# Optimization experiments

Hardware: AMD Instinct MI355X
Metric: run time of the kernel (lower is better)

The kernel has to match this reference:

```python
import jax, jax.numpy as jnp
import numpy as np
import math

B, H, S, D = 2, 16, 2048, 64

def setup_inputs() -> dict:
    key = jax.random.key(0)
    kq, kk, kv, km = jax.random.split(key, 4)
    query = jax.random.normal(kq, (B, H, S, D), dtype=jnp.float32)
    k_ = jax.random.normal(kk, (B, H, S, D), dtype=jnp.float32)
    value = jax.random.normal(kv, (B, H, S, D), dtype=jnp.float32)
    mask = jax.random.randint(km, (B, 1, 1, S), 0, 2, dtype=jnp.int32)
    return {"query": query, "key": k_, "value": value, "mask": mask}

def reference(query, key, value, mask):
    # scores: [B,H,S,S] = QK^T / sqrt(D)
    scale = 1.0 / math.sqrt(query.shape[-1])
    scores = jnp.einsum('bhqd,bhkd->bhqk', query, key) * scale
    # masked_fill(mask == 0, -1e9); mask broadcasts [B,1,1,S] -> [B,H,S,S]
    scores = jnp.where(mask == 0, jnp.float32(-1e9), scores)
    p_attn = jax.nn.softmax(scores, axis=-1)
    out = jnp.einsum('bhqk,bhkd->bhqd', p_attn, value)
    return (out, p_attn)
```

## Files before the change

kernel.cpp:

```cpp
#include <hip/hip_runtime.h>
#include <cstdint>
#include <cstddef>


typedef float f32x4 __attribute__((ext_vector_type(4)));
typedef short s16x8 __attribute__((ext_vector_type(8)));
typedef unsigned int u32;

#define S_LEN 2048
#define D_DIM 64
#define NKT   32
#define QSCALE 0.18033688011112042f

__device__ __forceinline__ unsigned short f2bf(float f) {
  unsigned u = __builtin_bit_cast(unsigned, f);
  u += 0x7FFFu + ((u >> 16) & 1u);
  return (unsigned short)(u >> 16);
}

__device__ __forceinline__ f32x4 mfma16(s16x8 a, s16x8 b, f32x4 c) {
  return __builtin_amdgcn_mfma_f32_16x16x32_bf16(a, b, c, 0, 0, 0);
}

__device__ __forceinline__ void gl_lds16(const void* g, void* l) {
  __builtin_amdgcn_global_load_lds(
      (const __attribute__((address_space(1))) u32*)g,
      (__attribute__((address_space(3))) u32*)l, 16, 0, 0);
}


__global__ void prep_k(const float* __restrict__ Kg, unsigned short* __restrict__ kb) {
  const int kt = blockIdx.x, bh = blockIdx.y, tid = threadIdx.x;
  const int r = tid >> 2, c0 = (tid & 3) << 4;
  const float* src = Kg + (((size_t)bh * S_LEN) + kt * 64 + r) * D_DIM + c0;
  f32x4 f0 = *(const f32x4*)(src);
  f32x4 f1 = *(const f32x4*)(src + 4);
  f32x4 f2 = *(const f32x4*)(src + 8);
  f32x4 f3 = *(const f32x4*)(src + 12);
  s16x8 h0, h1;
#pragma unroll
  for (int j = 0; j < 4; j++) {
    h0[j] = (short)f2bf(f0[j]); h0[j + 4] = (short)f2bf(f1[j]);
    h1[j] = (short)f2bf(f2[j]); h1[j + 4] = (short)f2bf(f3[j]);
  }
  char* dst = (char*)(kb + ((size_t)bh * 32 + kt) * 4096);
  const int swz = (r & 7) << 4;
  *(s16x8*)(dst + (r << 7) + (((c0 << 1) + 0)  ^ swz)) = h0;
  *(s16x8*)(dst + (r << 7) + (((c0 << 1) + 16) ^ swz)) = h1;
}

__global__ void prep_v(const float* __restrict__ Vg, unsigned short* __restrict__ vb) {
  __shared__ float tv[64 * 65];
  const int kt = blockIdx.x, bh = blockIdx.y, tid = threadIdx.x;
  const int r = tid >> 2, c0 = (tid & 3) << 4;
  const float* src = Vg + (((size_t)bh * S_LEN) + kt * 64 + r) * D_DIM + c0;
#pragma unroll
  for (int j = 0; j < 4; j++)
    *(f32x4*)(tv + r * 65 + c0 + j * 4) = *(const f32x4*)(src + j * 4);
  __syncthreads();
  const int d = tid >> 2, k0 = (tid & 3) << 4;
  s16x8 h0, h1;
#pragma unroll
  for (int j = 0; j < 8; j++) {
    h0[j] = (short)f2bf(tv[(k0 + j) * 65 + d]);
    h1[j] = (short)f2bf(tv[(k0 + 8 + j) * 65 + d]);
  }
  char* dst = (char*)(vb + ((size_t)bh * 32 + kt) * 4096);
  const int swz = (d & 7) << 4;
  *(s16x8*)(dst + (d << 7) + (((k0 << 1) + 0)  ^ swz)) = h0;
  *(s16x8*)(dst + (d << 7) + (((k0 << 1) + 16) ^ swz)) = h1;
}


__global__ __launch_bounds__(512, 4) void attn_main(
    const float* __restrict__ Qg, const unsigned short* __restrict__ Kb,
    const unsigned short* __restrict__ Vb, const int* __restrict__ Mg,
    float* __restrict__ Og, float* __restrict__ Pg)
{
  __shared__ __align__(16) short s_kv[4][4096];
  __shared__ __align__(16) short s_vv[4][4096];
  __shared__ __align__(16) short s_p[8][1024];

  const int tid = threadIdx.x;
  const int w = tid >> 6, l = tid & 63, lo = l & 15, hi = l >> 4;
  const int wg = blockIdx.x;
  const int bh = (wg & 7) * 4 + ((wg >> 3) >> 4);
  const int qt = (wg >> 3) & 15;
  const int b = bh >> 4;
  const int ph = wg & 31;

  unsigned* mbuild = (unsigned*)s_p;
  if (tid < 64) mbuild[tid] = 0u;
  __syncthreads();
  {
    const int4 mv = *(const int4*)(Mg + b * S_LEN + tid * 4);
    unsigned nib = (mv.x ? 1u : 0u) | (mv.y ? 2u : 0u) |
                   (mv.z ? 4u : 0u) | (mv.w ? 8u : 0u);
    atomicOr(&mbuild[tid >> 3], nib << ((tid & 7) * 4));
  }
  __syncthreads();
  const unsigned mword = mbuild[l];
  __syncthreads();

  const size_t bhS = (size_t)bh * S_LEN;
  const int q0w = qt * 128 + w * 16;

  const float* qsrc = Qg + (bhS + q0w + lo) * D_DIM + hi * 8;
  s16x8 bq0, bq1;
  {
    f32x4 a0 = *(const f32x4*)(qsrc);
    f32x4 a1 = *(const f32x4*)(qsrc + 4);
    f32x4 c0 = *(const f32x4*)(qsrc + 32);
    f32x4 c1 = *(const f32x4*)(qsrc + 36);
#pragma unroll
    for (int j = 0; j < 4; j++) {
      bq0[j]     = (short)f2bf(a0[j] * QSCALE);
      bq0[j + 4] = (short)f2bf(a1[j] * QSCALE);
      bq1[j]     = (short)f2bf(c0[j] * QSCALE);
      bq1[j + 4] = (short)f2bf(c1[j] * QSCALE);
    }
  }

  const char* ktile = (const char*)(Kb + bhS * D_DIM);
  const char* vtile = (const char*)(Vb + bhS * D_DIM);
  char* ldsk = (char*)s_kv;
  char* ldsv = (char*)s_vv;
  char* pb  = (char*)s_p[w];
  const int swz = (lo & 7) << 4;
  const int hs  = hi << 2;

  gl_lds16(ktile + ((0 + ph) & 31) * 8192 + tid * 16, ldsk + 0 * 8192 + tid * 16);
  gl_lds16(ktile + ((1 + ph) & 31) * 8192 + tid * 16, ldsk + 1 * 8192 + tid * 16);

  float lacc[4] = {0.f, 0.f, 0.f, 0.f};
  for (int j = 0; j < 16; j++) {
    const int h = j & 1;
    asm volatile("s_waitcnt vmcnt(0)" ::: "memory");
    __builtin_amdgcn_s_barrier();
    __builtin_amdgcn_sched_barrier(0);
    if (j < 15) {
      gl_lds16(ktile + ((2 * j + 2 + ph) & 31) * 8192 + tid * 16,
               ldsk + (2 * (h ^ 1)) * 8192 + tid * 16);
      gl_lds16(ktile + ((2 * j + 3 + ph) & 31) * 8192 + tid * 16,
               ldsk + (2 * (h ^ 1) + 1) * 8192 + tid * 16);
    }
#pragma unroll
    for (int t2 = 0; t2 < 2; t2++) {
      const int t = (2 * j + t2 + ph) & 31;
      const char* kc = ldsk + (2 * h + t2) * 8192;
      f32x4 acc[4] = {};
#pragma unroll
      for (int nn = 0; nn < 4; nn++) {
        const int rb = (nn * 16 + lo) << 7;
        s16x8 ka0 = *(const s16x8*)(kc + rb + ((0 + hi * 16) ^ swz));
        s16x8 ka1 = *(const s16x8*)(kc + rb + ((64 + hi * 16) ^ swz));
        acc[nn] = mfma16(ka0, bq0, acc[nn]);
        acc[nn] = mfma16(ka1, bq1, acc[nn]);
      }
      const unsigned w0 = (unsigned)__shfl((int)mword, 2 * t);
      const unsigned w1 = (unsigned)__shfl((int)mword, 2 * t + 1);
#pragma unroll
      for (int nn = 0; nn < 4; nn++) {
        const unsigned m4 = (((nn & 2) ? w1 : w0) >> (((nn & 1) << 4) + hs)) & 0xF;
#pragma unroll
        for (int r = 0; r < 4; r++) {
          const float e = exp2f(acc[nn][r]);
          lacc[nn] += ((m4 >> r) & 1) ? e : 0.0f;
        }
      }
    }
  }
  float lsum = (lacc[0] + lacc[1]) + (lacc[2] + lacc[3]);
  lsum += __shfl_xor(lsum, 16, 64);
  lsum += __shfl_xor(lsum, 32, 64);
  const float inv = 1.0f / lsum;

  __syncthreads();

  gl_lds16(ktile + ((0 + ph) & 31) * 8192 + tid * 16, ldsk + 0 * 8192 + tid * 16);
  gl_lds16(ktile + ((1 + ph) & 31) * 8192 + tid * 16, ldsk + 1 * 8192 + tid * 16);
  gl_lds16(vtile + ((0 + ph) & 31) * 8192 + tid * 16, ldsv + 0 * 8192 + tid * 16);
  gl_lds16(vtile + ((1 + ph) & 31) * 8192 + tid * 16, ldsv + 1 * 8192 + tid * 16);

  f32x4 oacc[4] = {};
  for (int j = 0; j < 16; j++) {
    const int h = j & 1;
    if (j == 0) asm volatile("s_waitcnt vmcnt(0)" ::: "memory");
    else        asm volatile("s_waitcnt vmcnt(8)" ::: "memory");
    __builtin_amdgcn_s_barrier();
    __builtin_amdgcn_sched_barrier(0);
    if (j < 15) {
      gl_lds16(ktile + ((2 * j + 2 + ph) & 31) * 8192 + tid * 16,
               ldsk + (2 * (h ^ 1)) * 8192 + tid * 16);
      gl_lds16(ktile + ((2 * j + 3 + ph) & 31) * 8192 + tid * 16,
               ldsk + (2 * (h ^ 1) + 1) * 8192 + tid * 16);
      gl_lds16(vtile + ((2 * j + 2 + ph) & 31) * 8192 + tid * 16,
               ldsv + (2 * (h ^ 1)) * 8192 + tid * 16);
      gl_lds16(vtile + ((2 * j + 3 + ph) & 31) * 8192 + tid * 16,
               ldsv + (2 * (h ^ 1) + 1) * 8192 + tid * 16);
    }
#pragma unroll
    for (int t2 = 0; t2 < 2; t2++) {
      const int t = (2 * j + t2 + ph) & 31;
      const char* kc = ldsk + (2 * h + t2) * 8192;
      const char* vc = ldsv + (2 * h + t2) * 8192;

      f32x4 acc[4] = {};
#pragma unroll
      for (int nn = 0; nn < 4; nn++) {
        const int rb = (nn * 16 + lo) << 7;
        s16x8 ka0 = *(const s16x8*)(kc + rb + ((0 + hi * 16) ^ swz));
        s16x8 ka1 = *(const s16x8*)(kc + rb + ((64 + hi * 16) ^ swz));
        acc[nn] = mfma16(ka0, bq0, acc[nn]);
        acc[nn] = mfma16(ka1, bq1, acc[nn]);
      }
      const unsigned w0 = (unsigned)__shfl((int)mword, 2 * t);
      const unsigned w1 = (unsigned)__shfl((int)mword, 2 * t + 1);
      const int colb = t * 64;
      float* prow = Pg + (bhS + q0w + lo) * S_LEN + colb;
#pragma unroll
      for (int nn = 0; nn < 4; nn++) {
        const unsigned m4 = (((nn & 2) ? w1 : w0) >> (((nn & 1) << 4) + hs)) & 0xF;
        f32x4 p;
#pragma unroll
        for (int r = 0; r < 4; r++) {
          const float e = exp2f(acc[nn][r]) * inv;
          p[r] = ((m4 >> r) & 1) ? e : 0.0f;
        }
        *(f32x4*)(prow + nn * 16 + hi * 4) = p;
        unsigned d0, d1;
        asm("v_cvt_pk_bf16_f32 %0, %1, %2" : "=v"(d0) : "v"(p[0]), "v"(p[1]));
        asm("v_cvt_pk_bf16_f32 %0, %1, %2" : "=v"(d1) : "v"(p[2]), "v"(p[3]));
        *(unsigned long long*)(pb + (lo << 7) + ((nn * 32 + hi * 8) ^ swz)) =
            ((unsigned long long)d1 << 32) | d0;
      }
#pragma unroll
      for (int kk2 = 0; kk2 < 2; kk2++) {
        s16x8 bp = *(const s16x8*)(pb + (lo << 7) + ((kk2 * 64 + hi * 16) ^ swz));
#pragma unroll
        for (int dd = 0; dd < 4; dd++) {
          s16x8 va = *(const s16x8*)(vc + ((dd * 16 + lo) << 7) +
                                     ((kk2 * 64 + hi * 16) ^ swz));
          oacc[dd] = mfma16(va, bp, oacc[dd]);
        }
      }
    }
  }
#pragma unroll
  for (int dd = 0; dd < 4; dd++)
    *(f32x4*)(Og + (bhS + q0w + lo) * D_DIM + dd * 16 + hi * 4) = oacc[dd];
}


__device__ __forceinline__ void stage_k(const float* __restrict__ g, char* lb, int tid) {
  const int kr = tid >> 2;
  const int c0 = (tid & 3) << 4;
  const f32x4* src = (const f32x4*)(g + kr * D_DIM + c0);
  f32x4 f0 = src[0], f1 = src[1], f2 = src[2], f3 = src[3];
  s16x8 h0, h1;
#pragma unroll
  for (int j = 0; j < 4; j++) {
    h0[j] = (short)f2bf(f0[j]); h0[j + 4] = (short)f2bf(f1[j]);
    h1[j] = (short)f2bf(f2[j]); h1[j + 4] = (short)f2bf(f3[j]);
  }
  const int base = kr << 7;
  const int swz = (kr & 7) << 4;
  *(s16x8*)(lb + base + (((c0 << 1) + 0) ^ swz)) = h0;
  *(s16x8*)(lb + base + (((c0 << 1) + 16) ^ swz)) = h1;
}

__device__ __forceinline__ void stage_v(const float* __restrict__ g, char* lb, int tid) {
  const int k0 = (tid >> 3) << 1;
  const int c0 = (tid & 7) << 3;
  const f32x4* s0 = (const f32x4*)(g + k0 * D_DIM + c0);
  const f32x4* s1 = (const f32x4*)(g + (k0 + 1) * D_DIM + c0);
  f32x4 a0 = s0[0], a1 = s0[1];
  f32x4 b0 = s1[0], b1 = s1[1];
  const int kc = (k0 >> 3) & 7;
  const int kb2 = (k0 & 7) << 1;
#pragma unroll
  for (int j = 0; j < 8; j++) {
    float fa = (j < 4) ? a0[j & 3] : a1[j & 3];
    float fb = (j < 4) ? b0[j & 3] : b1[j & 3];
    unsigned u = (unsigned)f2bf(fa) | ((unsigned)f2bf(fb) << 16);
    const int d = c0 + j;
    const int off = (d << 7) + (((kc ^ j ^ (d >> 3)) & 7) << 4) + kb2;
    *(unsigned*)(lb + off) = u;
  }
}

__global__ __launch_bounds__(256, 4) void attn_fwd(
    const float* __restrict__ Qg, const float* __restrict__ Kg,
    const float* __restrict__ Vg, const int* __restrict__ Mg,
    float* __restrict__ Og, float* __restrict__ Pg)
{
  __shared__ __align__(16) float s_bias[S_LEN];
  __shared__ __align__(16) short s_k[64 * 64];
  __shared__ __align__(16) short s_v[64 * 64];
  __shared__ __align__(16) short s_p[4 * 16 * 64];

  const int tid = threadIdx.x;
  const int w = tid >> 6, l = tid & 63, lo = l & 15, hi = l >> 4;
  const int bh = blockIdx.x, qt = blockIdx.y, b = bh >> 4;

  for (int i = tid; i < S_LEN; i += 256)
    s_bias[i] = Mg[b * S_LEN + i] ? 0.0f : -INFINITY;

  const int q0 = qt * 64 + w * 16;
  const float* qptr = Qg + ((size_t)bh * S_LEN + q0 + lo) * D_DIM + hi * 8;
  s16x8 aq[2];
#pragma unroll
  for (int kk = 0; kk < 2; kk++) {
    f32x4 v0 = *(const f32x4*)(qptr + kk * 32);
    f32x4 v1 = *(const f32x4*)(qptr + kk * 32 + 4);
#pragma unroll
    for (int j = 0; j < 4; j++) {
      aq[kk][j] = (short)f2bf(v0[j] * QSCALE);
      aq[kk][j + 4] = (short)f2bf(v1[j] * QSCALE);
    }
  }
  char* kb = (char*)s_k;
  char* vb = (char*)s_v;
  char* pb = (char*)s_p + (w << 11);
  const size_t bhS = (size_t)bh * S_LEN;
  __syncthreads();

  float lsum[4] = {0.f, 0.f, 0.f, 0.f};
  for (int kt = 0; kt < NKT; kt++) {
    stage_k(Kg + (bhS + kt * 64) * D_DIM, kb, tid);
    __syncthreads();
    f32x4 acc[4] = {};
#pragma unroll
    for (int kk = 0; kk < 2; kk++)
#pragma unroll
      for (int nn = 0; nn < 4; nn++) {
        const int row = nn * 16 + lo;
        s16x8 bk = *(const s16x8*)(kb + (row << 7) +
                     ((kk * 64 + hi * 16) ^ ((row & 7) << 4)));
        acc[nn] = mfma16(aq[kk], bk, acc[nn]);
      }
    const int colb = kt * 64;
#pragma unroll
    for (int nn = 0; nn < 4; nn++) {
      const float bias = s_bias[colb + nn * 16 + lo];
#pragma unroll
      for (int r = 0; r < 4; r++)
        lsum[r] += exp2f(acc[nn][r] + bias);
    }
    __syncthreads();
  }
#pragma unroll
  for (int r = 0; r < 4; r++)
#pragma unroll
    for (int off = 1; off < 16; off <<= 1)
      lsum[r] += __shfl_xor(lsum[r], off, 64);
  float inv[4];
#pragma unroll
  for (int r = 0; r < 4; r++) inv[r] = 1.0f / lsum[r];

  f32x4 oacc[4] = {};
  const int qd0 = q0 + hi * 4;
  for (int kt = 0; kt < NKT; kt++) {
    stage_k(Kg + (bhS + kt * 64) * D_DIM, kb, tid);
    stage_v(Vg + (bhS + kt * 64) * D_DIM, vb, tid);
    __syncthreads();
    f32x4 acc[4] = {};
#pragma unroll
    for (int kk = 0; kk < 2; kk++)
#pragma unroll
      for (int nn = 0; nn < 4; nn++) {
        const int row = nn * 16 + lo;
        s16x8 bk = *(const s16x8*)(kb + (row << 7) +
                     ((kk * 64 + hi * 16) ^ ((row & 7) << 4)));
        acc[nn] = mfma16(aq[kk], bk, acc[nn]);
      }
    const int colb = kt * 64;
#pragma unroll
    for (int nn = 0; nn < 4; nn++) {
      const int col = colb + nn * 16 + lo;
      const float bias = s_bias[col];
#pragma unroll
      for (int r = 0; r < 4; r++) {
        const float p = exp2f(acc[nn][r] + bias) * inv[r];
        Pg[(bhS + (size_t)(qd0 + r)) * S_LEN + col] = p;
        const int prow = hi * 4 + r;
        *(unsigned short*)(pb + (prow << 7) +
            ((((nn * 16 + lo) << 1)) ^ ((prow & 7) << 4))) = f2bf(p);
      }
    }
#pragma unroll
    for (int kk2 = 0; kk2 < 2; kk2++) {
      s16x8 ap = *(const s16x8*)(pb + (lo << 7) +
                   ((kk2 * 64 + hi * 16) ^ ((lo & 7) << 4)));
#pragma unroll
      for (int dd = 0; dd < 4; dd++) {
        const int d = dd * 16 + lo;
        const int chunk = ((kk2 * 4 + hi) ^ (d & 7) ^ (d >> 3)) & 7;
        s16x8 bv = *(const s16x8*)(vb + (d << 7) + (chunk << 4));
        oacc[dd] = mfma16(ap, bv, oacc[dd]);
      }
    }
    __syncthreads();
  }
#pragma unroll
  for (int dd = 0; dd < 4; dd++)
#pragma unroll
    for (int r = 0; r < 4; r++)
      Og[(bhS + (size_t)(qd0 + r)) * D_DIM + dd * 16 + lo] = oacc[dd][r];
}

extern "C" void kernel_launch(void* const* d_in, const int* in_sizes, int n_in,
                              void* d_out, int out_size, void* d_ws, size_t ws_size,
                              hipStream_t stream) {
  const float* Q = (const float*)d_in[0];
  const float* K = (const float*)d_in[1];
  const float* V = (const float*)d_in[2];
  const int*   M = (const int*)d_in[3];
  float* out = (float*)d_out;
  float* P = out + (size_t)2 * 16 * 2048 * 64;

  const size_t elems = (size_t)2 * 16 * 2048 * 64;
  if (ws_size >= elems * 2 * sizeof(unsigned short)) {
    unsigned short* kb = (unsigned short*)d_ws;
    unsigned short* vb = kb + elems;
    prep_k<<<dim3(32, 32), 256, 0, stream>>>(K, kb);
    prep_v<<<dim3(32, 32), 256, 0, stream>>>(V, vb);
    attn_main<<<dim3(512), 512, 0, stream>>>(Q, kb, vb, M, out, P);
  } else {
    attn_fwd<<<dim3(32, 32), dim3(256), 0, stream>>>(Q, K, V, M, out, P);
  }
}
```

Measured before the change: 177.7 us.

## Halve workgroup to 4 waves, each wave computing 32 query rows

The attention kernel now launches 256 threads per block instead of 512. Each wave handles 32 query rows (two 16-row MFMA tiles) instead of 16, so every K/V fragment read from LDS is reused across twice as many MFMAs. The K/V staging issues two global-to-LDS loads per thread per tile, the mask bitfield build is adapted, and the vmcnt wait counts are raised to match. In exchange there are fewer waves per block to hide latency and register pressure per wave goes up.

```diff
diff --git a/kernel.cpp b/kernel.cpp
--- a/kernel.cpp
+++ b/kernel.cpp
@@ -72,14 +72,25 @@
 }
 
 
-__global__ __launch_bounds__(512, 4) void attn_main(
+#define KSTAGE(t, buf) do { \
+    gl_lds16(ktile + (size_t)(t) * 8192 + tid * 16, \
+             ldsk + (buf) * 8192 + tid * 16); \
+    gl_lds16(ktile + (size_t)(t) * 8192 + 4096 + tid * 16, \
+             ldsk + (buf) * 8192 + 4096 + tid * 16); } while (0)
+#define VSTAGE(t, buf) do { \
+    gl_lds16(vtile + (size_t)(t) * 8192 + tid * 16, \
+             ldsv + (buf) * 8192 + tid * 16); \
+    gl_lds16(vtile + (size_t)(t) * 8192 + 4096 + tid * 16, \
+             ldsv + (buf) * 8192 + 4096 + tid * 16); } while (0)
+
+__global__ __launch_bounds__(256, 2) void attn_main(
     const float* __restrict__ Qg, const unsigned short* __restrict__ Kb,
     const unsigned short* __restrict__ Vb, const int* __restrict__ Mg,
     float* __restrict__ Og, float* __restrict__ Pg)
 {
   __shared__ __align__(16) short s_kv[4][4096];
   __shared__ __align__(16) short s_vv[4][4096];
-  __shared__ __align__(16) short s_p[8][1024];
+  __shared__ __align__(16) short s_p[4][2048];
 
   const int tid = threadIdx.x;
   const int w = tid >> 6, l = tid & 63, lo = l & 15, hi = l >> 4;
@@ -93,31 +104,37 @@
   if (tid < 64) mbuild[tid] = 0u;
   __syncthreads();
   {
-    const int4 mv = *(const int4*)(Mg + b * S_LEN + tid * 4);
-    unsigned nib = (mv.x ? 1u : 0u) | (mv.y ? 2u : 0u) |
-                   (mv.z ? 4u : 0u) | (mv.w ? 8u : 0u);
-    atomicOr(&mbuild[tid >> 3], nib << ((tid & 7) * 4));
+    const int4 m0 = *(const int4*)(Mg + b * S_LEN + tid * 8);
+    const int4 m1 = *(const int4*)(Mg + b * S_LEN + tid * 8 + 4);
+    unsigned byt =
+        (m0.x ? 1u : 0u) | (m0.y ? 2u : 0u) | (m0.z ? 4u : 0u) | (m0.w ? 8u : 0u) |
+        (m1.x ? 16u : 0u) | (m1.y ? 32u : 0u) | (m1.z ? 64u : 0u) | (m1.w ? 128u : 0u);
+    atomicOr(&mbuild[tid >> 2], byt << ((tid & 3) * 8));
   }
   __syncthreads();
   const unsigned mword = mbuild[l];
   __syncthreads();
 
   const size_t bhS = (size_t)bh * S_LEN;
-  const int q0w = qt * 128 + w * 16;
+  const int q0w = qt * 128 + w * 32;
 
   const float* qsrc = Qg + (bhS + q0w + lo) * D_DIM + hi * 8;
-  s16x8 bq0, bq1;
+  s16x8 bq0, bq1, bq2, bq3;
   {
     f32x4 a0 = *(const f32x4*)(qsrc);
     f32x4 a1 = *(const f32x4*)(qsrc + 4);
-    f32x4 c0 = *(const f32x4*)(qsrc + 32);
-    f32x4 c1 = *(const f32x4*)(qsrc + 36);
+    f32x4 a2 = *(const f32x4*)(qsrc + 32);
+    f32x4 a3 = *(const f32x4*)(qsrc + 36);
+    f32x4 c0 = *(const f32x4*)(qsrc + 1024);
+    f32x4 c1 = *(const f32x4*)(qsrc + 1028);
+    f32x4 c2 = *(const f32x4*)(qsrc + 1056);
+    f32x4 c3 = *(const f32x4*)(qsrc + 1060);
 #pragma unroll
     for (int j = 0; j < 4; j++) {
-      bq0[j]     = (short)f2bf(a0[j] * QSCALE);
-      bq0[j + 4] = (short)f2bf(a1[j] * QSCALE);
-      bq1[j]     = (short)f2bf(c0[j] * QSCALE);
-      bq1[j + 4] = (short)f2bf(c1[j] * QSCALE);
+      bq0[j] = (short)f2bf(a0[j] * QSCALE); bq0[j + 4] = (short)f2bf(a1[j] * QSCALE);
+      bq1[j] = (short)f2bf(a2[j] * QSCALE); bq1[j + 4] = (short)f2bf(a3[j] * QSCALE);
+      bq2[j] = (short)f2bf(c0[j] * QSCALE); bq2[j + 4] = (short)f2bf(c1[j] * QSCALE);
+      bq3[j] = (short)f2bf(c2[j] * QSCALE); bq3[j + 4] = (short)f2bf(c3[j] * QSCALE);
     }
   }
 
@@ -129,33 +146,34 @@
   const int swz = (lo & 7) << 4;
   const int hs  = hi << 2;
 
-  gl_lds16(ktile + ((0 + ph) & 31) * 8192 + tid * 16, ldsk + 0 * 8192 + tid * 16);
-  gl_lds16(ktile + ((1 + ph) & 31) * 8192 + tid * 16, ldsk + 1 * 8192 + tid * 16);
-
-  float lacc[4] = {0.f, 0.f, 0.f, 0.f};
+  KSTAGE((0 + ph) & 31, 0);
+  KSTAGE((1 + ph) & 31, 1);
+
+  float la0[4] = {0.f, 0.f, 0.f, 0.f};
+  float la1[4] = {0.f, 0.f, 0.f, 0.f};
   for (int j = 0; j < 16; j++) {
     const int h = j & 1;
     asm volatile("s_waitcnt vmcnt(0)" ::: "memory");
     __builtin_amdgcn_s_barrier();
     __builtin_amdgcn_sched_barrier(0);
     if (j < 15) {
-      gl_lds16(ktile + ((2 * j + 2 + ph) & 31) * 8192 + tid * 16,
-               ldsk + (2 * (h ^ 1)) * 8192 + tid * 16);
-      gl_lds16(ktile + ((2 * j + 3 + ph) & 31) * 8192 + tid * 16,
-               ldsk + (2 * (h ^ 1) + 1) * 8192 + tid * 16);
+      KSTAGE((2 * j + 2 + ph) & 31, 2 * (h ^ 1));
+      KSTAGE((2 * j + 3 + ph) & 31, 2 * (h ^ 1) + 1);
     }
 #pragma unroll
     for (int t2 = 0; t2 < 2; t2++) {
       const int t = (2 * j + t2 + ph) & 31;
       const char* kc = ldsk + (2 * h + t2) * 8192;
-      f32x4 acc[4] = {};
+      f32x4 a0[4] = {}, a1[4] = {};
 #pragma unroll
       for (int nn = 0; nn < 4; nn++) {
         const int rb = (nn * 16 + lo) << 7;
         s16x8 ka0 = *(const s16x8*)(kc + rb + ((0 + hi * 16) ^ swz));
         s16x8 ka1 = *(const s16x8*)(kc + rb + ((64 + hi * 16) ^ swz));
-        acc[nn] = mfma16(ka0, bq0, acc[nn]);
-        acc[nn] = mfma16(ka1, bq1, acc[nn]);
+        a0[nn] = mfma16(ka0, bq0, a0[nn]);
+        a0[nn] = mfma16(ka1, bq1, a0[nn]);
+        a1[nn] = mfma16(ka0, bq2, a1[nn]);
+        a1[nn] = mfma16(ka1, bq3, a1[nn]);
       }
       const unsigned w0 = (unsigned)__shfl((int)mword, 2 * t);
       const unsigned w1 = (unsigned)__shfl((int)mword, 2 * t + 1);
@@ -164,40 +182,42 @@
         const unsigned m4 = (((nn & 2) ? w1 : w0) >> (((nn & 1) << 4) + hs)) & 0xF;
 #pragma unroll
         for (int r = 0; r < 4; r++) {
-          const float e = exp2f(acc[nn][r]);
-          lacc[nn] += ((m4 >> r) & 1) ? e : 0.0f;
+          const float e0 = exp2f(a0[nn][r]);
+          const float e1 = exp2f(a1[nn][r]);
+          la0[nn] += ((m4 >> r) & 1) ? e0 : 0.0f;
+          la1[nn] += ((m4 >> r) & 1) ? e1 : 0.0f;
         }
       }
     }
   }
-  float lsum = (lacc[0] + lacc[1]) + (lacc[2] + lacc[3]);
-  lsum += __shfl_xor(lsum, 16, 64);
-  lsum += __shfl_xor(lsum, 32, 64);
-  const float inv = 1.0f / lsum;
-
-  __syncthreads();
-
-  gl_lds16(ktile + ((0 + ph) & 31) * 8192 + tid * 16, ldsk + 0 * 8192 + tid * 16);
-  gl_lds16(ktile + ((1 + ph) & 31) * 8192 + tid * 16, ldsk + 1 * 8192 + tid * 16);
-  gl_lds16(vtile + ((0 + ph) & 31) * 8192 + tid * 16, ldsv + 0 * 8192 + tid * 16);
-  gl_lds16(vtile + ((1 + ph) & 31) * 8192 + tid * 16, ldsv + 1 * 8192 + tid * 16);
-
-  f32x4 oacc[4] = {};
+  float lsum0 = (la0[0] + la0[1]) + (la0[2] + la0[3]);
+  float lsum1 = (la1[0] + la1[1]) + (la1[2] + la1[3]);
+  lsum0 += __shfl_xor(lsum0, 16, 64);
+  lsum0 += __shfl_xor(lsum0, 32, 64);
+  lsum1 += __shfl_xor(lsum1, 16, 64);
+  lsum1 += __shfl_xor(lsum1, 32, 64);
+  const float inv0 = 1.0f / lsum0;
+  const float inv1 = 1.0f / lsum1;
+
+  __syncthreads();
+
+  KSTAGE((0 + ph) & 31, 0);
+  KSTAGE((1 + ph) & 31, 1);
+  VSTAGE((0 + ph) & 31, 0);
+  VSTAGE((1 + ph) & 31, 1);
+
+  f32x4 o0[4] = {}, o1[4] = {};
   for (int j = 0; j < 16; j++) {
     const int h = j & 1;
     if (j == 0) asm volatile("s_waitcnt vmcnt(0)" ::: "memory");
-    else        asm volatile("s_waitcnt vmcnt(8)" ::: "memory");
+    else        asm volatile("s_waitcnt vmcnt(16)" ::: "memory");
     __builtin_amdgcn_s_barrier();
     __builtin_amdgcn_sched_barrier(0);
     if (j < 15) {
-      gl_lds16(ktile + ((2 * j + 2 + ph) & 31) * 8192 + tid * 16,
-               ldsk + (2 * (h ^ 1)) * 8192 + tid * 16);
-      gl_lds16(ktile + ((2 * j + 3 + ph) & 31) * 8192 + tid * 16,
-               ldsk + (2 * (h ^ 1) + 1) * 8192 + tid * 16);
-      gl_lds16(vtile + ((2 * j + 2 + ph) & 31) * 8192 + tid * 16,
-               ldsv + (2 * (h ^ 1)) * 8192 + tid * 16);
-      gl_lds16(vtile + ((2 * j + 3 + ph) & 31) * 8192 + tid * 16,
-               ldsv + (2 * (h ^ 1) + 1) * 8192 + tid * 16);
+      KSTAGE((2 * j + 2 + ph) & 31, 2 * (h ^ 1));
+      KSTAGE((2 * j + 3 + ph) & 31, 2 * (h ^ 1) + 1);
+      VSTAGE((2 * j + 2 + ph) & 31, 2 * (h ^ 1));
+      VSTAGE((2 * j + 3 + ph) & 31, 2 * (h ^ 1) + 1);
     }
 #pragma unroll
     for (int t2 = 0; t2 < 2; t2++) {
@@ -205,50 +225,66 @@
       const char* kc = ldsk + (2 * h + t2) * 8192;
       const char* vc = ldsv + (2 * h + t2) * 8192;
 
-      f32x4 acc[4] = {};
+      f32x4 a0[4] = {}, a1[4] = {};
 #pragma unroll
       for (int nn = 0; nn < 4; nn++) {
         const int rb = (nn * 16 + lo) << 7;
         s16x8 ka0 = *(const s16x8*)(kc + rb + ((0 + hi * 16) ^ swz));
         s16x8 ka1 = *(const s16x8*)(kc + rb + ((64 + hi * 16) ^ swz));
-        acc[nn] = mfma16(ka0, bq0, acc[nn]);
-        acc[nn] = mfma16(ka1, bq1, acc[nn]);
+        a0[nn] = mfma16(ka0, bq0, a0[nn]);
+        a0[nn] = mfma16(ka1, bq1, a0[nn]);
+        a1[nn] = mfma16(ka0, bq2, a1[nn]);
+        a1[nn] = mfma16(ka1, bq3, a1[nn]);
       }
       const unsigned w0 = (unsigned)__shfl((int)mword, 2 * t);
       const unsigned w1 = (unsigned)__shfl((int)mword, 2 * t + 1);
       const int colb = t * 64;
-      float* prow = Pg + (bhS + q0w + lo) * S_LEN + colb;
+      float* prow0 = Pg + (bhS + q0w + lo) * S_LEN + colb;
+      float* prow1 = prow0 + 16 * S_LEN;
 #pragma unroll
       for (int nn = 0; nn < 4; nn++) {
         const unsigned m4 = (((nn & 2) ? w1 : w0) >> (((nn & 1) << 4) + hs)) & 0xF;
-        f32x4 p;
+        f32x4 p0, p1;
 #pragma unroll
         for (int r = 0; r < 4; r++) {
-          const float e = exp2f(acc[nn][r]) * inv;
-          p[r] = ((m4 >> r) & 1) ? e : 0.0f;
+          const float e0 = exp2f(a0[nn][r]) * inv0;
+          const float e1 = exp2f(a1[nn][r]) * inv1;
+          p0[r] = ((m4 >> r) & 1) ? e0 : 0.0f;
+          p1[r] = ((m4 >> r) & 1) ? e1 : 0.0f;
         }
-        *(f32x4*)(prow + nn * 16 + hi * 4) = p;
-        unsigned d0, d1;
-        asm("v_cvt_pk_bf16_f32 %0, %1, %2" : "=v"(d0) : "v"(p[0]), "v"(p[1]));
-        asm("v_cvt_pk_bf16_f32 %0, %1, %2" : "=v"(d1) : "v"(p[2]), "v"(p[3]));
-        *(unsigned long long*)(pb + (lo << 7) + ((nn * 32 + hi * 8) ^ swz)) =
+        *(f32x4*)(prow0 + nn * 16 + hi * 4) = p0;
+        *(f32x4*)(prow1 + nn * 16 + hi * 4) = p1;
+        unsigned d0, d1, d2, d3;
+        asm("v_cvt_pk_bf16_f32 %0, %1, %2" : "=v"(d0) : "v"(p0[0]), "v"(p0[1]));
+        asm("v_cvt_pk_bf16_f32 %0, %1, %2" : "=v"(d1) : "v"(p0[2]), "v"(p0[3]));
+        asm("v_cvt_pk_bf16_f32 %0, %1, %2" : "=v"(d2) : "v"(p1[0]), "v"(p1[1]));
+        asm("v_cvt_pk_bf16_f32 %0, %1, %2" : "=v"(d3) : "v"(p1[2]), "v"(p1[3]));
+        const int boff = (lo << 7) + ((nn * 32 + hi * 8) ^ swz);
+        *(unsigned long long*)(pb + boff) =
             ((unsigned long long)d1 << 32) | d0;
+        *(unsigned long long*)(pb + 2048 + boff) =
+            ((unsigned long long)d3 << 32) | d2;
       }
 #pragma unroll
       for (int kk2 = 0; kk2 < 2; kk2++) {
-        s16x8 bp = *(const s16x8*)(pb + (lo << 7) + ((kk2 * 64 + hi * 16) ^ swz));
+        const int poff = (lo << 7) + ((kk2 * 64 + hi * 16) ^ swz);
+        s16x8 bp0 = *(const s16x8*)(pb + poff);
+        s16x8 bp1 = *(const s16x8*)(pb + 2048 + poff);
 #pragma unroll
         for (int dd = 0; dd < 4; dd++) {
           s16x8 va = *(const s16x8*)(vc + ((dd * 16 + lo) << 7) +
                                      ((kk2 * 64 + hi * 16) ^ swz));
-          oacc[dd] = mfma16(va, bp, oacc[dd]);
+          o0[dd] = mfma16(va, bp0, o0[dd]);
+          o1[dd] = mfma16(va, bp1, o1[dd]);
         }
       }
     }
   }
 #pragma unroll
-  for (int dd = 0; dd < 4; dd++)
-    *(f32x4*)(Og + (bhS + q0w + lo) * D_DIM + dd * 16 + hi * 4) = oacc[dd];
+  for (int dd = 0; dd < 4; dd++) {
+    *(f32x4*)(Og + (bhS + q0w + lo) * D_DIM + dd * 16 + hi * 4) = o0[dd];
+    *(f32x4*)(Og + (bhS + q0w + 16 + lo) * D_DIM + dd * 16 + hi * 4) = o1[dd];
+  }
 }
 
 
@@ -425,7 +461,7 @@
     unsigned short* vb = kb + elems;
     prep_k<<<dim3(32, 32), 256, 0, stream>>>(K, kb);
     prep_v<<<dim3(32, 32), 256, 0, stream>>>(V, vb);
-    attn_main<<<dim3(512), 512, 0, stream>>>(Q, kb, vb, M, out, P);
+    attn_main<<<dim3(512), 256, 0, stream>>>(Q, kb, vb, M, out, P);
   } else {
     attn_fwd<<<dim3(32, 32), dim3(256), 0, stream>>>(Q, K, V, M, out, P);
   }
```

After: 199.5 us. 1.12x slower.

## Merge K/V prep kernels and deepen pass-1 K tile prefetch to four tiles

Applied to the files above, without the earlier changes.

The separate K and V bf16 conversion kernels become one launch that uses a z-dimension of 2, which removes one kernel launch and lets both conversions run at the same time. The first (row-sum) pass of the attention kernel now loads four K tiles per step into a unified 64KB LDS buffer instead of two, which halves the number of barrier and wait iterations. The second pass reuses the same buffer split into K and V halves. LDS use per block stays the same because the two buffers are merged, and each prefetch group is larger.

```diff
diff --git a/kernel.cpp b/kernel.cpp
--- a/kernel.cpp
+++ b/kernel.cpp
@@ -28,47 +28,45 @@
       (__attribute__((address_space(3))) u32*)l, 16, 0, 0);
 }
 
-
-__global__ void prep_k(const float* __restrict__ Kg, unsigned short* __restrict__ kb) {
-  const int kt = blockIdx.x, bh = blockIdx.y, tid = threadIdx.x;
-  const int r = tid >> 2, c0 = (tid & 3) << 4;
-  const float* src = Kg + (((size_t)bh * S_LEN) + kt * 64 + r) * D_DIM + c0;
-  f32x4 f0 = *(const f32x4*)(src);
-  f32x4 f1 = *(const f32x4*)(src + 4);
-  f32x4 f2 = *(const f32x4*)(src + 8);
-  f32x4 f3 = *(const f32x4*)(src + 12);
-  s16x8 h0, h1;
-#pragma unroll
-  for (int j = 0; j < 4; j++) {
-    h0[j] = (short)f2bf(f0[j]); h0[j + 4] = (short)f2bf(f1[j]);
-    h1[j] = (short)f2bf(f2[j]); h1[j + 4] = (short)f2bf(f3[j]);
-  }
-  char* dst = (char*)(kb + ((size_t)bh * 32 + kt) * 4096);
-  const int swz = (r & 7) << 4;
-  *(s16x8*)(dst + (r << 7) + (((c0 << 1) + 0)  ^ swz)) = h0;
-  *(s16x8*)(dst + (r << 7) + (((c0 << 1) + 16) ^ swz)) = h1;
-}
-
-__global__ void prep_v(const float* __restrict__ Vg, unsigned short* __restrict__ vb) {
+__global__ void prep_kv(const float* __restrict__ Kg, const float* __restrict__ Vg,
+                        unsigned short* __restrict__ kb, unsigned short* __restrict__ vb) {
   __shared__ float tv[64 * 65];
   const int kt = blockIdx.x, bh = blockIdx.y, tid = threadIdx.x;
   const int r = tid >> 2, c0 = (tid & 3) << 4;
-  const float* src = Vg + (((size_t)bh * S_LEN) + kt * 64 + r) * D_DIM + c0;
-#pragma unroll
-  for (int j = 0; j < 4; j++)
-    *(f32x4*)(tv + r * 65 + c0 + j * 4) = *(const f32x4*)(src + j * 4);
-  __syncthreads();
-  const int d = tid >> 2, k0 = (tid & 3) << 4;
-  s16x8 h0, h1;
-#pragma unroll
-  for (int j = 0; j < 8; j++) {
-    h0[j] = (short)f2bf(tv[(k0 + j) * 65 + d]);
-    h1[j] = (short)f2bf(tv[(k0 + 8 + j) * 65 + d]);
-  }
-  char* dst = (char*)(vb + ((size_t)bh * 32 + kt) * 4096);
-  const int swz = (d & 7) << 4;
-  *(s16x8*)(dst + (d << 7) + (((k0 << 1) + 0)  ^ swz)) = h0;
-  *(s16x8*)(dst + (d << 7) + (((k0 << 1) + 16) ^ swz)) = h1;
+  if (blockIdx.z == 0) {
+    const float* src = Kg + (((size_t)bh * S_LEN) + kt * 64 + r) * D_DIM + c0;
+    f32x4 f0 = *(const f32x4*)(src);
+    f32x4 f1 = *(const f32x4*)(src + 4);
+    f32x4 f2 = *(const f32x4*)(src + 8);
+    f32x4 f3 = *(const f32x4*)(src + 12);
+    s16x8 h0, h1;
+#pragma unroll
+    for (int j = 0; j < 4; j++) {
+      h0[j] = (short)f2bf(f0[j]); h0[j + 4] = (short)f2bf(f1[j]);
+      h1[j] = (short)f2bf(f2[j]); h1[j + 4] = (short)f2bf(f3[j]);
+    }
+    char* dst = (char*)(kb + ((size_t)bh * 32 + kt) * 4096);
+    const int swz = (r & 7) << 4;
+    *(s16x8*)(dst + (r << 7) + (((c0 << 1) + 0)  ^ swz)) = h0;
+    *(s16x8*)(dst + (r << 7) + (((c0 << 1) + 16) ^ swz)) = h1;
+  } else {
+    const float* src = Vg + (((size_t)bh * S_LEN) + kt * 64 + r) * D_DIM + c0;
+#pragma unroll
+    for (int j = 0; j < 4; j++)
+      *(f32x4*)(tv + r * 65 + c0 + j * 4) = *(const f32x4*)(src + j * 4);
+    __syncthreads();
+    const int d = tid >> 2, k0 = (tid & 3) << 4;
+    s16x8 h0, h1;
+#pragma unroll
+    for (int j = 0; j < 8; j++) {
+      h0[j] = (short)f2bf(tv[(k0 + j) * 65 + d]);
+      h1[j] = (short)f2bf(tv[(k0 + 8 + j) * 65 + d]);
+    }
+    char* dst = (char*)(vb + ((size_t)bh * 32 + kt) * 4096);
+    const int swz = (d & 7) << 4;
+    *(s16x8*)(dst + (d << 7) + (((k0 << 1) + 0)  ^ swz)) = h0;
+    *(s16x8*)(dst + (d << 7) + (((k0 << 1) + 16) ^ swz)) = h1;
+  }
 }
 
 
@@ -77,8 +75,7 @@
     const unsigned short* __restrict__ Vb, const int* __restrict__ Mg,
     float* __restrict__ Og, float* __restrict__ Pg)
 {
-  __shared__ __align__(16) short s_kv[4][4096];
-  __shared__ __align__(16) short s_vv[4][4096];
+  __shared__ __align__(16) short s_kv[8][4096];
   __shared__ __align__(16) short s_p[8][1024];
 
   const int tid = threadIdx.x;
@@ -123,31 +120,34 @@
 
   const char* ktile = (const char*)(Kb + bhS * D_DIM);
   const char* vtile = (const char*)(Vb + bhS * D_DIM);
-  char* ldsk = (char*)s_kv;
-  char* ldsv = (char*)s_vv;
+  char* base = (char*)s_kv;
   char* pb  = (char*)s_p[w];
   const int swz = (lo & 7) << 4;
   const int hs  = hi << 2;
 
-  gl_lds16(ktile + ((0 + ph) & 31) * 8192 + tid * 16, ldsk + 0 * 8192 + tid * 16);
-  gl_lds16(ktile + ((1 + ph) & 31) * 8192 + tid * 16, ldsk + 1 * 8192 + tid * 16);
+  gl_lds16(ktile + ((0 + ph) & 31) * 8192 + tid * 16, base + 0 * 8192 + tid * 16);
+  gl_lds16(ktile + ((1 + ph) & 31) * 8192 + tid * 16, base + 1 * 8192 + tid * 16);
+  gl_lds16(ktile + ((2 + ph) & 31) * 8192 + tid * 16, base + 2 * 8192 + tid * 16);
+  gl_lds16(ktile + ((3 + ph) & 31) * 8192 + tid * 16, base + 3 * 8192 + tid * 16);
 
   float lacc[4] = {0.f, 0.f, 0.f, 0.f};
-  for (int j = 0; j < 16; j++) {
+  for (int j = 0; j < 8; j++) {
     const int h = j & 1;
     asm volatile("s_waitcnt vmcnt(0)" ::: "memory");
     __builtin_amdgcn_s_barrier();
     __builtin_amdgcn_sched_barrier(0);
-    if (j < 15) {
-      gl_lds16(ktile + ((2 * j + 2 + ph) & 31) * 8192 + tid * 16,
-               ldsk + (2 * (h ^ 1)) * 8192 + tid * 16);
-      gl_lds16(ktile + ((2 * j + 3 + ph) & 31) * 8192 + tid * 16,
-               ldsk + (2 * (h ^ 1) + 1) * 8192 + tid * 16);
-    }
-#pragma unroll
-    for (int t2 = 0; t2 < 2; t2++) {
-      const int t = (2 * j + t2 + ph) & 31;
-      const char* kc = ldsk + (2 * h + t2) * 8192;
+    if (j < 7) {
+      const int tb = 4 * j + 4;
+      char* dst = base + (h ^ 1) * 32768;
+      gl_lds16(ktile + ((tb + 0 + ph) & 31) * 8192 + tid * 16, dst + 0 * 8192 + tid * 16);
+      gl_lds16(ktile + ((tb + 1 + ph) & 31) * 8192 + tid * 16, dst + 1 * 8192 + tid * 16);
+      gl_lds16(ktile + ((tb + 2 + ph) & 31) * 8192 + tid * 16, dst + 2 * 8192 + tid * 16);
+      gl_lds16(ktile + ((tb + 3 + ph) & 31) * 8192 + tid * 16, dst + 3 * 8192 + tid * 16);
+    }
+#pragma unroll
+    for (int t2 = 0; t2 < 4; t2++) {
+      const int t = (4 * j + t2 + ph) & 31;
+      const char* kc = base + h * 32768 + t2 * 8192;
       f32x4 acc[4] = {};
 #pragma unroll
       for (int nn = 0; nn < 4; nn++) {
@@ -177,6 +177,8 @@
 
   __syncthreads();
 
+  char* ldsk = base;
+  char* ldsv = base + 32768;
   gl_lds16(ktile + ((0 + ph) & 31) * 8192 + tid * 16, ldsk + 0 * 8192 + tid * 16);
   gl_lds16(ktile + ((1 + ph) & 31) * 8192 + tid * 16, ldsk + 1 * 8192 + tid * 16);
   gl_lds16(vtile + ((0 + ph) & 31) * 8192 + tid * 16, ldsv + 0 * 8192 + tid * 16);
@@ -423,8 +425,7 @@
   if (ws_size >= elems * 2 * sizeof(unsigned short)) {
     unsigned short* kb = (unsigned short*)d_ws;
     unsigned short* vb = kb + elems;
-    prep_k<<<dim3(32, 32), 256, 0, stream>>>(K, kb);
-    prep_v<<<dim3(32, 32), 256, 0, stream>>>(V, vb);
+    prep_kv<<<dim3(32, 32, 2), 256, 0, stream>>>(K, V, kb, vb);
     attn_main<<<dim3(512), 512, 0, stream>>>(Q, kb, vb, M, out, P);
   } else {
     attn_fwd<<<dim3(32, 32), dim3(256), 0, stream>>>(Q, K, V, M, out, P);
```

New measurement: 172.4 us. 3.0% less time.
